# Kernel tuning notes

Hardware: AMD Instinct MI355X
Metric: run time of the kernel (lower is better)

## Reference

```python
import jax, jax.numpy as jnp
import numpy as np

L = 5          # num_layer
D = 256        # emb_dim
N = 50000      # nodes
E = 800000     # edges
NUM_ATOM_FEATS, ATOM_VOCAB = 9, 120
NUM_BOND_FEATS, BOND_VOCAB = 3, 6
BN_EPS = 1e-5


def setup_inputs() -> dict:
    key = jax.random.key(0)
    ks = jax.random.split(key, 16)
    s = 0.02
    inp = {
        "x": jax.random.randint(ks[0], (N, NUM_ATOM_FEATS), 0, ATOM_VOCAB),
        "edge_index": jax.random.randint(ks[1], (2, E), 0, N),
        "edge_attr": jax.random.randint(ks[2], (E, NUM_BOND_FEATS), 0, BOND_VOCAB),
        "atom_emb": jax.random.normal(ks[3], (NUM_ATOM_FEATS, ATOM_VOCAB, D), jnp.float32) * s,
        "bond_emb": jax.random.normal(ks[4], (L, NUM_BOND_FEATS, BOND_VOCAB, D), jnp.float32) * s,
        "eps": jnp.zeros((L,), jnp.float32),
        "W1": jax.random.normal(ks[5], (L, D, 2 * D), jnp.float32) * s,
        "b1": jnp.zeros((L, 2 * D), jnp.float32),
        "g1": jnp.ones((L, 2 * D), jnp.float32),
        "be1": jnp.zeros((L, 2 * D), jnp.float32),
        "W2": jax.random.normal(ks[6], (L, 2 * D, D), jnp.float32) * s,
        "b2": jnp.zeros((L, D), jnp.float32),
        "g2": jnp.ones((L, D), jnp.float32),
        "be2": jnp.zeros((L, D), jnp.float32),
    }
    return inp


def _batchnorm(h, g, b):
    # training-mode BatchNorm1d over the node dimension
    m = jnp.mean(h, axis=0)
    v = jnp.mean(jnp.square(h - m), axis=0)
    return (h - m) * jax.lax.rsqrt(v + BN_EPS) * g + b


def reference(x, edge_index, edge_attr, atom_emb, bond_emb, eps,
              W1, b1, g1, be1, W2, b2, g2, be2):
    # AtomEncoder: sum of per-feature embedding lookups -> [N, D]
    h = jnp.sum(
        jnp.stack([atom_emb[f][x[:, f]] for f in range(NUM_ATOM_FEATS)], 0), 0)
    src, dst = edge_index[0], edge_index[1]
    for l in range(L):
        # BondEncoder for this layer -> [E, D]
        e = jnp.sum(jnp.stack(
            [bond_emb[l, f][edge_attr[:, f]] for f in range(NUM_BOND_FEATS)], 0), 0)
        msg = jax.nn.relu(h[src] + e)                          # gather + transform
        agg = jax.ops.segment_sum(msg, dst, num_segments=N)   # scatter-add
        z = (1.0 + eps[l]) * h + agg
        z = _batchnorm(z @ W1[l] + b1[l], g1[l], be1[l])       # MLP hidden + BN
        z = jax.nn.relu(z) @ W2[l] + b2[l]
        z = _batchnorm(z, g2[l], be2[l])                       # outer BN
        if l < L - 1:
            z = jax.nn.relu(z)
        h = z
    return h  # JK='last', drop_ratio=0
```

## Files before the change

kernel.cpp:

```cpp
#include <hip/hip_runtime.h>
#include <stdint.h>

#define NODES 50000
#define EDGES 800000
#define EMB   256
#define MPAD  50048
#define BNEPS 1e-5f
#define SCANB 196

typedef unsigned short u16;
typedef unsigned int   u32;
typedef _Float16 f16;
typedef __attribute__((ext_vector_type(4))) _Float16 f16x4;
typedef __attribute__((ext_vector_type(8))) _Float16 f16x8;
typedef __attribute__((ext_vector_type(4))) float f32x4;

__device__ __forceinline__ void gload16(const void* g, void* l){
  __builtin_amdgcn_global_load_lds((const __attribute__((address_space(1))) void*)g,
                                   (__attribute__((address_space(3))) void*)l, 16, 0, 0);
}


__global__ void k_w1t(const float* __restrict__ W1, f16* __restrict__ Wt){
  int i = blockIdx.x * 256 + threadIdx.x;
  if (i >= 5*512*256) return;
  int k = i & 255, n = (i >> 8) & 511, l = i >> 17;
  Wt[i] = (f16)W1[((size_t)l << 17) + ((size_t)k << 9) + n];
}
__global__ void k_w2t(const float* __restrict__ W2, f16* __restrict__ Wt){
  int i = blockIdx.x * 256 + threadIdx.x;
  if (i >= 5*256*512) return;
  int k = i & 511, n = (i >> 9) & 255, l = i >> 17;
  Wt[i] = (f16)W2[((size_t)l << 17) + ((size_t)k << 8) + n];
}

__global__ void k_ebond(const float* __restrict__ bemb, f16* __restrict__ eb){
  int l = blockIdx.x / 216, p = blockIdx.x % 216;
  int a0 = p % 6, a1 = (p / 6) % 6, a2 = p / 36;
  int d0 = threadIdx.x * 4;
  const float* b = bemb + (size_t)l * 3 * 6 * 256;
  float4 v0 = *(const float4*)(b + (0*6 + a0)*256 + d0);
  float4 v1 = *(const float4*)(b + (1*6 + a1)*256 + d0);
  float4 v2 = *(const float4*)(b + (2*6 + a2)*256 + d0);
  f16x4 o = {(f16)(v0.x+v1.x+v2.x), (f16)(v0.y+v1.y+v2.y),
             (f16)(v0.z+v1.z+v2.z), (f16)(v0.w+v1.w+v2.w)};
  *(f16x4*)(eb + (((size_t)l*216 + p) << 8) + d0) = o;
}

__global__ void k_atom(const int* __restrict__ x, const float* __restrict__ aemb,
                       f16* __restrict__ h){
  int n = blockIdx.x * 4 + (threadIdx.x >> 6);
  int lane = threadIdx.x & 63;
  if (n >= NODES) return;
  int d0 = lane * 4;
  float a0=0.f, a1=0.f, a2=0.f, a3=0.f;
#pragma unroll
  for (int f = 0; f < 9; ++f){
    int v = x[n*9 + f];
    float4 e = *(const float4*)(aemb + (((size_t)f*120 + v) << 8) + d0);
    a0 += e.x; a1 += e.y; a2 += e.z; a3 += e.w;
  }
  f16x4 o = {(f16)a0, (f16)a1, (f16)a2, (f16)a3};
  *(f16x4*)(h + (size_t)n*EMB + d0) = o;
}


__global__ void k_hist(const int* __restrict__ dst, int* __restrict__ counts){
  int e = blockIdx.x * 256 + threadIdx.x;
  if (e < EDGES) atomicAdd(&counts[dst[e]], 1);
}

__global__ void k_bsum(const int* __restrict__ counts, int* __restrict__ bsums){
  __shared__ int red[256];
  int t = threadIdx.x;
  int i = blockIdx.x * 256 + t;
  red[t] = (i < NODES) ? counts[i] : 0;
  __syncthreads();
  for (int off = 128; off > 0; off >>= 1){
    if (t < off) red[t] += red[t + off];
    __syncthreads();
  }
  if (t == 0) bsums[blockIdx.x] = red[0];
}

__global__ void k_bscan(int* __restrict__ bsums){
  __shared__ int sc[256];
  int t = threadIdx.x;
  int v = (t < SCANB) ? bsums[t] : 0;
  sc[t] = v;
  __syncthreads();
  for (int off = 1; off < 256; off <<= 1){
    int u = (t >= off) ? sc[t - off] : 0;
    __syncthreads();
    sc[t] += u;
    __syncthreads();
  }
  if (t < SCANB) bsums[t] = sc[t] - v;
}

__global__ void k_fill(const int* __restrict__ counts, const int* __restrict__ bsums,
                       int* __restrict__ rs, int* __restrict__ fill){
  __shared__ int sc[256];
  int t = threadIdx.x;
  int i = blockIdx.x * 256 + t;
  int v = (i < NODES) ? counts[i] : 0;
  sc[t] = v;
  __syncthreads();
  for (int off = 1; off < 256; off <<= 1){
    int u = (t >= off) ? sc[t - off] : 0;
    __syncthreads();
    sc[t] += u;
    __syncthreads();
  }
  if (i < NODES){
    int e = bsums[blockIdx.x] + sc[t] - v;
    rs[i] = e; fill[i] = e;
    if (i == NODES - 1) rs[NODES] = e + v;
  }
}

__global__ void k_scatter(const int* __restrict__ src, const int* __restrict__ dst,
                          const int* __restrict__ ea, int* __restrict__ fill,
                          int* __restrict__ csrc, int* __restrict__ cattr){
  int e = blockIdx.x * 256 + threadIdx.x;
  if (e >= EDGES) return;
  int d = dst[e];
  int p = atomicAdd(&fill[d], 1);
  csrc[p]  = src[e];
  cattr[p] = ea[e*3+0] + 6*ea[e*3+1] + 36*ea[e*3+2];
}


__global__ void k_gather(const f16* __restrict__ h, const f16* __restrict__ ebl,
                         const int* __restrict__ rs, const int* __restrict__ csrc,
                         const int* __restrict__ cattr, const float* __restrict__ epsv,
                         int layer, f16* __restrict__ z){
  int n = blockIdx.x * 4 + (threadIdx.x >> 6);
  int lane = threadIdx.x & 63;
  int half = lane >> 5;
  int dl = (lane & 31) * 8;
  if (n >= MPAD) return;
  if (n >= NODES){
    if (half == 0){
      f16x8 zz = {(f16)0.f,(f16)0.f,(f16)0.f,(f16)0.f,(f16)0.f,(f16)0.f,(f16)0.f,(f16)0.f};
      *(f16x8*)(z + (size_t)n*EMB + dl) = zz;
    }
    return;
  }
  float acc[8];
#pragma unroll
  for (int k = 0; k < 8; ++k) acc[k] = 0.f;
  int i1 = rs[n+1];
  int i  = rs[n] + half;
  bool v = i < i1;
  int s = 0, pa = 0;
  if (v){ s = csrc[i]; pa = cattr[i]; }
  while (v){
    f16x8 hv = *(const f16x8*)(h + (size_t)s*EMB + dl);
    f16x8 ev = *(const f16x8*)(ebl + ((size_t)pa << 8) + dl);
    int in = i + 2;
    bool vn = in < i1;
    int sn = 0, pan = 0;
    if (vn){ sn = csrc[in]; pan = cattr[in]; }
#pragma unroll
    for (int k = 0; k < 8; ++k)
      acc[k] += fmaxf((float)hv[k] + (float)ev[k], 0.f);
    i = in; s = sn; pa = pan; v = vn;
  }
#pragma unroll
  for (int k = 0; k < 8; ++k) acc[k] += __shfl_xor(acc[k], 32);
  if (half == 0){
    float ep = 1.0f + epsv[layer];
    f16x8 hv = *(const f16x8*)(h + (size_t)n*EMB + dl);
    f16x8 o;
#pragma unroll
    for (int k = 0; k < 8; ++k) o[k] = (f16)(acc[k] + ep*(float)hv[k]);
    *(f16x8*)(z + (size_t)n*EMB + dl) = o;
  }
}

template<int K, int NCOL, bool FUSEBN>
__global__ __launch_bounds__(256)
void k_gemm(const f16* __restrict__ A, const f16* __restrict__ Bt,
            const f16* __restrict__ bnsc, const f16* __restrict__ bnsh,
            f16* __restrict__ C, float* __restrict__ csum, float* __restrict__ csq){
  __shared__ __align__(16) u16 As[128*64];
  __shared__ __align__(16) u16 Bs[128*64];
  const int tid  = threadIdx.x;
  const int lane = tid & 63;
  const int wid  = tid >> 6;
  const int bm0 = blockIdx.x * 128;
  const int bn0 = blockIdx.y * 128;
  const int wm = (wid >> 1) * 64;
  const int wn = (wid & 1) * 64;

  f32x4 acc[4][4];
#pragma unroll
  for (int m = 0; m < 4; ++m)
#pragma unroll
    for (int n = 0; n < 4; ++n) acc[m][n] = (f32x4){0.f,0.f,0.f,0.f};

  const f16x8 zero8 = {(f16)0.f,(f16)0.f,(f16)0.f,(f16)0.f,
                       (f16)0.f,(f16)0.f,(f16)0.f,(f16)0.f};

  for (int kt = 0; kt < K/64; ++kt){
    __syncthreads();
#pragma unroll
    for (int it = 0; it < 4; ++it){
      int tix = tid + it*256;
      int r = tix >> 3;
      int c = tix & 7;
      int sc = c ^ (r & 7);
      gload16(A  + (size_t)(bm0 + r)*K + kt*64 + sc*8, (char*)As + tix*16);
      gload16(Bt + (size_t)(bn0 + r)*K + kt*64 + sc*8, (char*)Bs + tix*16);
    }
    __syncthreads();
#pragma unroll
    for (int kk = 0; kk < 2; ++kk){
      f16x8 af[4], bfr[4];
#pragma unroll
      for (int m = 0; m < 4; ++m){
        int row = wm + m*16 + (lane & 15);
        int phys = (kk*4 + (lane >> 4)) ^ (row & 7);
        af[m] = *(const f16x8*)((const char*)As + row*128 + phys*16);
      }
#pragma unroll
      for (int n = 0; n < 4; ++n){
        int row = wn + n*16 + (lane & 15);
        int phys = (kk*4 + (lane >> 4)) ^ (row & 7);
        bfr[n] = *(const f16x8*)((const char*)Bs + row*128 + phys*16);
      }
      if (FUSEBN){
        int kb = kt*64 + (kk*4 + (lane >> 4))*8;
        f16x8 sc = *(const f16x8*)(bnsc + kb);
        f16x8 sh = *(const f16x8*)(bnsh + kb);
#pragma unroll
        for (int m = 0; m < 4; ++m){
          f16x8 t = af[m]*sc + sh;
#pragma unroll
          for (int j = 0; j < 8; ++j) t[j] = (t[j] > (f16)0.f) ? t[j] : (f16)0.f;
          af[m] = (bm0 + wm + m*16 + (lane & 15) < NODES) ? t : zero8;
        }
      }
#pragma unroll
      for (int m = 0; m < 4; ++m)
#pragma unroll
        for (int n = 0; n < 4; ++n)
          acc[m][n] = __builtin_amdgcn_mfma_f32_16x16x32_f16(af[m], bfr[n], acc[m][n], 0, 0, 0);
    }
  }

  const int r0 = (lane >> 4) * 4;
  const int cc = lane & 15;
#pragma unroll
  for (int m = 0; m < 4; ++m)
#pragma unroll
    for (int n = 0; n < 4; ++n)
#pragma unroll
      for (int j = 0; j < 4; ++j){
        int row = bm0 + wm + m*16 + r0 + j;
        int col = bn0 + wn + n*16 + cc;
        C[(size_t)row*NCOL + col] = (f16)acc[m][n][j];
      }
#pragma unroll
  for (int n = 0; n < 4; ++n){
    float s = 0.f, q = 0.f;
#pragma unroll
    for (int m = 0; m < 4; ++m)
#pragma unroll
      for (int j = 0; j < 4; ++j){ float v = acc[m][n][j]; s += v; q += v*v; }
    s += __shfl_xor(s, 16); q += __shfl_xor(q, 16);
    s += __shfl_xor(s, 32); q += __shfl_xor(q, 32);
    if (lane < 16){
      atomicAdd(csum + bn0 + wn + n*16 + cc, s);
      atomicAdd(csq  + bn0 + wn + n*16 + cc, q);
    }
  }
}

__global__ void k_finalize(const float* __restrict__ sum, const float* __restrict__ sumsq,
                           const float* __restrict__ g, const float* __restrict__ be,
                           float* __restrict__ scale, float* __restrict__ shift,
                           f16* __restrict__ scf, f16* __restrict__ shf, int nc){
  int c = blockIdx.x * 256 + threadIdx.x;
  if (c >= nc) return;
  float m = sum[c] * (1.0f / NODES);
  float v = sumsq[c] * (1.0f / NODES) - m*m;
  float sc = rsqrtf(v + BNEPS) * g[c];
  float sh = be[c] - m*sc;
  scale[c] = sc;  shift[c] = sh;
  scf[c] = (f16)sc;  shf[c] = (f16)sh;
}

__global__ void k_apply2(const f16* __restrict__ zp, const float* __restrict__ scale,
                         const float* __restrict__ shift, f16* __restrict__ hout,
                         float* __restrict__ fout, int dorelu){
  int idx = blockIdx.x * 256 + threadIdx.x;
  int row = idx >> 5;
  int c0  = (idx & 31) * 8;
  if (row >= NODES) return;
  size_t off = (size_t)row * EMB + c0;
  f16x8 v = *(const f16x8*)(zp + off);
  float4 sA = *(const float4*)(scale + c0), sB = *(const float4*)(scale + c0 + 4);
  float4 tA = *(const float4*)(shift + c0), tB = *(const float4*)(shift + c0 + 4);
  float r0 = (float)v[0]*sA.x + tA.x;
  float r1 = (float)v[1]*sA.y + tA.y;
  float r2 = (float)v[2]*sA.z + tA.z;
  float r3 = (float)v[3]*sA.w + tA.w;
  float r4 = (float)v[4]*sB.x + tB.x;
  float r5 = (float)v[5]*sB.y + tB.y;
  float r6 = (float)v[6]*sB.z + tB.z;
  float r7 = (float)v[7]*sB.w + tB.w;
  if (dorelu){
    r0=fmaxf(r0,0.f); r1=fmaxf(r1,0.f); r2=fmaxf(r2,0.f); r3=fmaxf(r3,0.f);
    r4=fmaxf(r4,0.f); r5=fmaxf(r5,0.f); r6=fmaxf(r6,0.f); r7=fmaxf(r7,0.f);
  }
  if (fout){
    float4 f0 = {r0,r1,r2,r3}, f1 = {r4,r5,r6,r7};
    float* q = fout + off;
    *(float4*)q = f0; *(float4*)(q + 4) = f1;
  } else {
    f16x8 o = {(f16)r0,(f16)r1,(f16)r2,(f16)r3,(f16)r4,(f16)r5,(f16)r6,(f16)r7};
    *(f16x8*)(hout + off) = o;
  }
}


extern "C" void kernel_launch(void* const* d_in, const int* in_sizes, int n_in,
                              void* d_out, int out_size, void* d_ws, size_t ws_size,
                              hipStream_t stream){
  const int*   x    = (const int*)  d_in[0];
  const int*   ei   = (const int*)  d_in[1];
  const int*   ea   = (const int*)  d_in[2];
  const float* aemb = (const float*)d_in[3];
  const float* bemb = (const float*)d_in[4];
  const float* epsv = (const float*)d_in[5];
  const float* W1   = (const float*)d_in[6];
  const float* g1   = (const float*)d_in[8];
  const float* be1  = (const float*)d_in[9];
  const float* W2   = (const float*)d_in[10];
  const float* g2   = (const float*)d_in[12];
  const float* be2  = (const float*)d_in[13];
  float* out = (float*)d_out;

  char* p = (char*)d_ws;
  auto take = [&](size_t bytes){ char* r = p; p += (bytes + 255) & ~(size_t)255; return r; };
  f16* h      = (f16*)take((size_t)NODES*EMB*2);
  f16* z      = (f16*)take((size_t)MPAD*EMB*2);
  f16* hidden = (f16*)take((size_t)MPAD*512*2);
  f16* W1t    = (f16*)take((size_t)5*512*256*2);
  f16* W2t    = (f16*)take((size_t)5*256*512*2);
  f16* eb     = (f16*)take((size_t)5*216*256*2);
  float* stats= (float*)take((size_t)4*512*4);
  float* csum = stats, *csq = stats + 512, *scale = stats + 1024, *shift = stats + 1536;
  f16* scf    = (f16*)take((size_t)512*2);
  f16* shf    = (f16*)take((size_t)512*2);
  int* counts = (int*)take((size_t)NODES*4);
  int* rs     = (int*)take((size_t)(NODES+1)*4);
  int* fill   = (int*)take((size_t)NODES*4);
  int* bsums  = (int*)take((size_t)SCANB*4);
  int* csrc   = (int*)take((size_t)EDGES*4);
  int* cattr  = (int*)take((size_t)EDGES*4);

  k_w1t<<<2560, 256, 0, stream>>>(W1, W1t);
  k_w2t<<<2560, 256, 0, stream>>>(W2, W2t);
  k_ebond<<<5*216, 64, 0, stream>>>(bemb, eb);
  k_atom<<<12500, 256, 0, stream>>>(x, aemb, h);
  hipMemsetAsync(counts, 0, (size_t)NODES*4, stream);
  k_hist<<<EDGES/256, 256, 0, stream>>>(ei + EDGES, counts);
  k_bsum<<<SCANB, 256, 0, stream>>>(counts, bsums);
  k_bscan<<<1, 256, 0, stream>>>(bsums);
  k_fill<<<SCANB, 256, 0, stream>>>(counts, bsums, rs, fill);
  k_scatter<<<EDGES/256, 256, 0, stream>>>(ei, ei + EDGES, ea, fill, csrc, cattr);

  for (int l = 0; l < 5; ++l){
    k_gather<<<MPAD/4, 256, 0, stream>>>(h, eb + (size_t)l*216*256, rs, csrc, cattr, epsv, l, z);
    hipMemsetAsync(stats, 0, 2*512*4, stream);
    k_gemm<256,512,false><<<dim3(MPAD/128, 4), 256, 0, stream>>>(
        z, W1t + (size_t)l*512*256, nullptr, nullptr, hidden, csum, csq);
    k_finalize<<<2, 256, 0, stream>>>(csum, csq, g1 + l*512, be1 + l*512,
                                      scale, shift, scf, shf, 512);
    hipMemsetAsync(stats, 0, 2*512*4, stream);
    k_gemm<512,256,true><<<dim3(MPAD/128, 2), 256, 0, stream>>>(
        hidden, W2t + (size_t)l*256*512, scf, shf, z, csum, csq);
    k_finalize<<<1, 256, 0, stream>>>(csum, csq, g2 + l*256, be2 + l*256,
                                      scale, shift, scf, shf, 256);
    if (l < 4)
      k_apply2<<<NODES*32/256, 256, 0, stream>>>(z, scale, shift, h, nullptr, 1);
    else
      k_apply2<<<NODES*32/256, 256, 0, stream>>>(z, scale, shift, nullptr, out, 0);
  }
}
```

Baseline: 1.188 ms.

## Double-buffer GEMM LDS tiles and replace global stat atomics with per-block partials

The GEMM kernel now double-buffers its A/B LDS tiles, so the next K-tile is loaded while MFMAs run on the current one, with a single wait and barrier per iteration. Column sum and sum-of-squares for batch norm are first reduced in shared memory and written as per-row-block partials instead of global atomics. The finalize kernel then sums the 391 partials per column, which removes the memsets. LDS use doubles, which may lower occupancy, and the serial 391-step loop in finalize runs on only a few blocks.

```diff
diff --git a/kernel.cpp b/kernel.cpp
--- a/kernel.cpp
+++ b/kernel.cpp
@@ -5,6 +5,7 @@
 #define EDGES 800000
 #define EMB   256
 #define MPAD  50048
+#define NBX   391
 #define BNEPS 1e-5f
 #define SCANB 196
 
@@ -183,9 +184,10 @@
 __global__ __launch_bounds__(256)
 void k_gemm(const f16* __restrict__ A, const f16* __restrict__ Bt,
             const f16* __restrict__ bnsc, const f16* __restrict__ bnsh,
-            f16* __restrict__ C, float* __restrict__ csum, float* __restrict__ csq){
-  __shared__ __align__(16) u16 As[128*64];
-  __shared__ __align__(16) u16 Bs[128*64];
+            f16* __restrict__ C, float* __restrict__ psum, float* __restrict__ psq){
+  __shared__ __align__(16) u16 As[2][128*64];
+  __shared__ __align__(16) u16 Bs[2][128*64];
+  __shared__ float red[2][128];
   const int tid  = threadIdx.x;
   const int lane = tid & 63;
   const int wid  = tid >> 6;
@@ -193,28 +195,36 @@
   const int bn0 = blockIdx.y * 128;
   const int wm = (wid >> 1) * 64;
   const int wn = (wid & 1) * 64;
-
-  f32x4 acc[4][4];
-#pragma unroll
-  for (int m = 0; m < 4; ++m)
-#pragma unroll
-    for (int n = 0; n < 4; ++n) acc[m][n] = (f32x4){0.f,0.f,0.f,0.f};
-
-  const f16x8 zero8 = {(f16)0.f,(f16)0.f,(f16)0.f,(f16)0.f,
-                       (f16)0.f,(f16)0.f,(f16)0.f,(f16)0.f};
-
-  for (int kt = 0; kt < K/64; ++kt){
-    __syncthreads();
+  const int NT = K/64;
+
+  auto STAGE = [&](int b, int kt){
 #pragma unroll
     for (int it = 0; it < 4; ++it){
       int tix = tid + it*256;
       int r = tix >> 3;
       int c = tix & 7;
       int sc = c ^ (r & 7);
-      gload16(A  + (size_t)(bm0 + r)*K + kt*64 + sc*8, (char*)As + tix*16);
-      gload16(Bt + (size_t)(bn0 + r)*K + kt*64 + sc*8, (char*)Bs + tix*16);
+      gload16(A  + (size_t)(bm0 + r)*K + kt*64 + sc*8, (char*)As[b] + tix*16);
+      gload16(Bt + (size_t)(bn0 + r)*K + kt*64 + sc*8, (char*)Bs[b] + tix*16);
     }
-    __syncthreads();
+  };
+
+  f32x4 acc[4][4];
+#pragma unroll
+  for (int m = 0; m < 4; ++m)
+#pragma unroll
+    for (int n = 0; n < 4; ++n) acc[m][n] = (f32x4){0.f,0.f,0.f,0.f};
+
+  const f16x8 zero8 = {(f16)0.f,(f16)0.f,(f16)0.f,(f16)0.f,
+                       (f16)0.f,(f16)0.f,(f16)0.f,(f16)0.f};
+
+  STAGE(0, 0);
+  asm volatile("s_waitcnt vmcnt(0)" ::: "memory");
+  __builtin_amdgcn_s_barrier();
+  int buf = 0;
+
+  for (int kt = 0; kt < NT; ++kt){
+    if (kt + 1 < NT) STAGE(buf ^ 1, kt + 1);
 #pragma unroll
     for (int kk = 0; kk < 2; ++kk){
       f16x8 af[4], bfr[4];
@@ -222,13 +232,13 @@
       for (int m = 0; m < 4; ++m){
         int row = wm + m*16 + (lane & 15);
         int phys = (kk*4 + (lane >> 4)) ^ (row & 7);
-        af[m] = *(const f16x8*)((const char*)As + row*128 + phys*16);
+        af[m] = *(const f16x8*)((const char*)As[buf] + row*128 + phys*16);
       }
 #pragma unroll
       for (int n = 0; n < 4; ++n){
         int row = wn + n*16 + (lane & 15);
         int phys = (kk*4 + (lane >> 4)) ^ (row & 7);
-        bfr[n] = *(const f16x8*)((const char*)Bs + row*128 + phys*16);
+        bfr[n] = *(const f16x8*)((const char*)Bs[buf] + row*128 + phys*16);
       }
       if (FUSEBN){
         int kb = kt*64 + (kk*4 + (lane >> 4))*8;
@@ -248,6 +258,9 @@
         for (int n = 0; n < 4; ++n)
           acc[m][n] = __builtin_amdgcn_mfma_f32_16x16x32_f16(af[m], bfr[n], acc[m][n], 0, 0, 0);
     }
+    asm volatile("s_waitcnt vmcnt(0)" ::: "memory");
+    __builtin_amdgcn_s_barrier();
+    buf ^= 1;
   }
 
   const int r0 = (lane >> 4) * 4;
@@ -262,6 +275,8 @@
         int col = bn0 + wn + n*16 + cc;
         C[(size_t)row*NCOL + col] = (f16)acc[m][n][j];
       }
+  if (tid < 128){ red[0][tid] = 0.f; red[1][tid] = 0.f; }
+  __syncthreads();
 #pragma unroll
   for (int n = 0; n < 4; ++n){
     float s = 0.f, q = 0.f;
@@ -272,20 +287,30 @@
     s += __shfl_xor(s, 16); q += __shfl_xor(q, 16);
     s += __shfl_xor(s, 32); q += __shfl_xor(q, 32);
     if (lane < 16){
-      atomicAdd(csum + bn0 + wn + n*16 + cc, s);
-      atomicAdd(csq  + bn0 + wn + n*16 + cc, q);
+      atomicAdd(&red[0][wn + n*16 + cc], s);
+      atomicAdd(&red[1][wn + n*16 + cc], q);
     }
   }
-}
-
-__global__ void k_finalize(const float* __restrict__ sum, const float* __restrict__ sumsq,
+  __syncthreads();
+  if (tid < 128){
+    psum[(size_t)blockIdx.x*NCOL + bn0 + tid] = red[0][tid];
+    psq [(size_t)blockIdx.x*NCOL + bn0 + tid] = red[1][tid];
+  }
+}
+
+__global__ void k_finalize(const float* __restrict__ psum, const float* __restrict__ psq,
                            const float* __restrict__ g, const float* __restrict__ be,
                            float* __restrict__ scale, float* __restrict__ shift,
                            f16* __restrict__ scf, f16* __restrict__ shf, int nc){
   int c = blockIdx.x * 256 + threadIdx.x;
   if (c >= nc) return;
-  float m = sum[c] * (1.0f / NODES);
-  float v = sumsq[c] * (1.0f / NODES) - m*m;
+  float s = 0.f, q = 0.f;
+  for (int b = 0; b < NBX; ++b){
+    s += psum[(size_t)b*nc + c];
+    q += psq [(size_t)b*nc + c];
+  }
+  float m = s * (1.0f / NODES);
+  float v = q * (1.0f / NODES) - m*m;
   float sc = rsqrtf(v + BNEPS) * g[c];
   float sh = be[c] - m*sc;
   scale[c] = sc;  shift[c] = sh;
@@ -351,8 +376,10 @@
   f16* W1t    = (f16*)take((size_t)5*512*256*2);
   f16* W2t    = (f16*)take((size_t)5*256*512*2);
   f16* eb     = (f16*)take((size_t)5*216*256*2);
-  float* stats= (float*)take((size_t)4*512*4);
-  float* csum = stats, *csq = stats + 512, *scale = stats + 1024, *shift = stats + 1536;
+  float* psum = (float*)take((size_t)NBX*512*4);
+  float* psq  = (float*)take((size_t)NBX*512*4);
+  float* scale= (float*)take((size_t)512*4);
+  float* shift= (float*)take((size_t)512*4);
   f16* scf    = (f16*)take((size_t)512*2);
   f16* shf    = (f16*)take((size_t)512*2);
   int* counts = (int*)take((size_t)NODES*4);
@@ -375,15 +402,13 @@
 
   for (int l = 0; l < 5; ++l){
     k_gather<<<MPAD/4, 256, 0, stream>>>(h, eb + (size_t)l*216*256, rs, csrc, cattr, epsv, l, z);
-    hipMemsetAsync(stats, 0, 2*512*4, stream);
-    k_gemm<256,512,false><<<dim3(MPAD/128, 4), 256, 0, stream>>>(
-        z, W1t + (size_t)l*512*256, nullptr, nullptr, hidden, csum, csq);
-    k_finalize<<<2, 256, 0, stream>>>(csum, csq, g1 + l*512, be1 + l*512,
+    k_gemm<256,512,false><<<dim3(NBX, 4), 256, 0, stream>>>(
+        z, W1t + (size_t)l*512*256, nullptr, nullptr, hidden, psum, psq);
+    k_finalize<<<2, 256, 0, stream>>>(psum, psq, g1 + l*512, be1 + l*512,
                                       scale, shift, scf, shf, 512);
-    hipMemsetAsync(stats, 0, 2*512*4, stream);
-    k_gemm<512,256,true><<<dim3(MPAD/128, 2), 256, 0, stream>>>(
-        hidden, W2t + (size_t)l*256*512, scf, shf, z, csum, csq);
-    k_finalize<<<1, 256, 0, stream>>>(csum, csq, g2 + l*256, be2 + l*256,
+    k_gemm<512,256,true><<<dim3(NBX, 2), 256, 0, stream>>>(
+        hidden, W2t + (size_t)l*256*512, scf, shf, z, psum, psq);
+    k_finalize<<<1, 256, 0, stream>>>(psum, psq, g2 + l*256, be2 + l*256,
                                       scale, shift, scf, shf, 256);
     if (l < 4)
       k_apply2<<<NODES*32/256, 256, 0, stream>>>(z, scale, shift, h, nullptr, 1);
```

New measurement: 1.495 ms. 25.9% more time.
